# Kernel tuning notes

Hardware: AMD Instinct MI355X
Metric: run time of the kernel (lower is better)

The kernel has to match this reference:

```python
import jax, jax.numpy as jnp
import numpy as np

D_MODEL = 5
NUM_PRED = 3
D_K = D_MODEL + NUM_PRED  # 8
HIDDEN = 128
GRID_LEN = 0.1
NUM_GRIDS = 100  # time_horizon / grid_length
SCALE = float(np.power(D_K, 0.5))
OH = np.eye(NUM_PRED, dtype=np.float32)
ONEHOT_M = jnp.asarray(OH[0])   # mental predicate 0
ONEHOT_A1 = jnp.asarray(OH[1])  # action predicate 1
ONEHOT_A2 = jnp.asarray(OH[2])  # action predicate 2


def time_emb(t):
    # positional-style embedding: even dims sin, odd dims cos (matches fast_time_embedding)
    i = jnp.arange(D_MODEL)
    ang = jnp.asarray(t)[..., None] / (10000.0 ** (2.0 * i / D_MODEL))
    return jnp.where(i % 2 == 0, jnp.sin(ang), jnp.cos(ang))


def setup_inputs() -> dict:
    key = jax.random.key(0)
    ks = jax.random.split(key, 11)
    B, L = 1024, 2048
    times_a1 = jnp.sort(jax.random.uniform(ks[0], (B, L)) * 10.0, axis=1)
    times_a2 = jnp.sort(jax.random.uniform(ks[1], (B, L)) * 10.0, axis=1)
    u = jax.random.uniform(ks[2], (B, NUM_GRIDS))
    s = 0.05
    return {
        'times_a1': times_a1,
        'times_a2': times_a2,
        'u': u,
        'W_ih': s * jax.random.normal(ks[3], (4 * HIDDEN, 21)),
        'W_hh': s * jax.random.normal(ks[4], (4 * HIDDEN, HIDDEN)),
        'b_ih': s * jax.random.normal(ks[5], (4 * HIDDEN,)),
        'b_hh': s * jax.random.normal(ks[6], (4 * HIDDEN,)),
        'w1': s * jax.random.normal(ks[7], (5, HIDDEN)),
        'b1': s * jax.random.normal(ks[8], (5,)),
        'w2': s * jax.random.normal(ks[9], (1, 5)),
        'b2': s * jax.random.normal(ks[10], (1,)),
    }


def _forward(times_a1, times_a2, u, W_ih, W_hh, b_ih, b_hh, w1, b1, w2, b2):
    B = times_a1.shape[0]
    # action event embeddings: [B, L, D_MODEL+NUM_PRED]; k = v = concat over action types
    e1 = jnp.concatenate([time_emb(times_a1), jnp.broadcast_to(ONEHOT_A1, times_a1.shape + (NUM_PRED,))], axis=-1)
    e2 = jnp.concatenate([time_emb(times_a2), jnp.broadcast_to(ONEHOT_A2, times_a2.shape + (NUM_PRED,))], axis=-1)
    kv = jnp.concatenate([e1, e2], axis=1)  # [B, 2L, 8]

    cur_times = (jnp.arange(NUM_GRIDS) + 1.0) * GRID_LEN  # [100]

    def step(carry, xs):
        hx, cx, last_time, has_event, dyn_time = carry
        cur_time, u_t = xs
        # query for mental predicate 0 at cur_time: [8]
        q = jnp.concatenate([time_emb(cur_time), ONEHOT_M])
        scores = jnp.einsum('d,bld->bl', q, kv) / SCALE
        attn = jax.nn.softmax(scores, axis=-1)
        att_out = jnp.einsum('bl,bld->bd', attn, kv)  # [B, 8]
        # mental embedding: zeros before first event, else time-emb of last event + one-hot
        m_emb = jnp.concatenate([time_emb(last_time), jnp.broadcast_to(ONEHOT_M, (B, NUM_PRED))], axis=-1)
        m_emb = jnp.where(has_event[:, None], m_emb, 0.0)
        dyn_time = dyn_time + GRID_LEN
        ct_emb = time_emb(dyn_time)  # [B, 5]
        x = jnp.concatenate([att_out, m_emb, ct_emb], axis=-1)  # [B, 21]
        # torch LSTMCell: gates ordered i, f, g, o
        gates = x @ W_ih.T + hx @ W_hh.T + b_ih + b_hh
        i_, f_, g_, o_ = jnp.split(gates, 4, axis=-1)
        cx = jax.nn.sigmoid(f_) * cx + jax.nn.sigmoid(i_) * jnp.tanh(g_)
        hx = jax.nn.sigmoid(o_) * jnp.tanh(cx)
        hz = jax.nn.sigmoid((hx @ w1.T + b1) @ w2.T + b2)[:, 0]  # [B]
        # bernoulli(prob) with pre-drawn uniform; single mental predicate -> index always 0
        event = u_t < hz
        last_time = jnp.where(event, cur_time, last_time)
        has_event = has_event | event
        dyn_time = jnp.where(event, 0.0, dyn_time)
        return (hx, cx, last_time, has_event, dyn_time), (hz, event)

    init = (
        jnp.zeros((B, HIDDEN)), jnp.zeros((B, HIDDEN)),
        jnp.zeros((B,)), jnp.zeros((B,), dtype=bool), jnp.zeros((B,)),
    )
    _, (hazard, events) = jax.lax.scan(step, init, (cur_times, u.T))
    return hazard, events  # [NUM_GRIDS, B], [NUM_GRIDS, B]


def reference(times_a1, times_a2, u, W_ih, W_hh, b_ih, b_hh, w1, b1, w2, b2):
    return _forward(times_a1, times_a2, u, W_ih, W_hh, b_ih, b_hh, w1, b1, w2, b2)
```

## Files before the change

### kernel.cpp

```cpp
#include <hip/hip_runtime.h>
#include <math.h>

#define BTOT 1024
#define LEN  2048
#define T    100
#define HID  128

#define C1 0.025118864315095794
#define C2 6.309573444801933e-04
#define C3 1.5848931924611134e-05
#define C4 3.9810717055349735e-07

#define TEMB(td) \
  float d0 = sinf((float)(td)); \
  float d1 = cosf((float)((td) * C1)); \
  float d2 = sinf((float)((td) * C2)); \
  float d3 = cosf((float)((td) * C3)); \
  float d4 = sinf((float)((td) * C4));

__device__ __forceinline__ float sig(float x) { return 1.0f / (1.0f + expf(-x)); }

using v2f = __attribute__((ext_vector_type(2))) float;
__device__ __forceinline__ v2f mkv2(float a, float b) { v2f r; r.x = a; r.y = b; return r; }

template <int CTRL>
__device__ __forceinline__ float dppadd(float x) {
  int r = __builtin_amdgcn_update_dpp(0, __float_as_int(x), CTRL, 0xF, 0xF, false);
  return x + __int_as_float(r);
}
__device__ __forceinline__ float wred(float x) {
  x = dppadd<0xB1>(x);
  x = dppadd<0x4E>(x);
  x = dppadd<0x124>(x);
  x = dppadd<0x128>(x);
  x += __shfl_xor(x, 16);
  x += __shfl_xor(x, 32);
  return x;
}
#define RED4(x) { x = dppadd<0xB1>(x); x = dppadd<0x4E>(x); }

#define AGSTASH(a_, v_) asm volatile("v_accvgpr_write_b32 %0, %1" : "=a"(a_) : "v"(v_))
#define AGREAD(v_, a_)  asm volatile("v_accvgpr_read_b32 %0, %1" : "=v"(v_) : "a"(a_))

__global__ __attribute__((amdgpu_flat_work_group_size(512, 512)))
void attn_k(const float* __restrict__ ta1,
            const float* __restrict__ ta2,
            float* __restrict__ att) {
  const int b = blockIdx.x, tid = threadIdx.x;
  const int wave = tid >> 6, lane = tid & 63;

  __shared__ float qlds[T][8];
  __shared__ float strip[8][T][8];

  if (tid < T) {
    double ct = (double)(tid + 1) * 0.1;
    TEMB(ct);
    qlds[tid][0] = d0 * 0.35355339059327373f;
    qlds[tid][1] = d1 * 0.35355339059327373f;
    qlds[tid][2] = d2 * 0.35355339059327373f;
    qlds[tid][3] = d3 * 0.35355339059327373f;
    qlds[tid][4] = d4 * 0.35355339059327373f;
  }

#define E5(i) float e##i##_0, e##i##_1, e##i##_2, e##i##_3, e##i##_4;
  E5(0) E5(1) E5(2) E5(3) E5(4) E5(5) E5(6) E5(7)
#undef E5
#define STAGE(i, expr) { double td_ = (double)(expr); \
    e##i##_0 = sinf((float)td_); \
    e##i##_1 = cosf((float)(td_ * C1)); \
    e##i##_2 = sinf((float)(td_ * C2)); \
    e##i##_3 = cosf((float)(td_ * C3)); \
    e##i##_4 = sinf((float)(td_ * C4)); }
  STAGE(0, ta1[b * LEN + tid +    0])
  STAGE(1, ta1[b * LEN + tid +  512])
  STAGE(2, ta1[b * LEN + tid + 1024])
  STAGE(3, ta1[b * LEN + tid + 1536])
  STAGE(4, ta2[b * LEN + tid +    0])
  STAGE(5, ta2[b * LEN + tid +  512])
  STAGE(6, ta2[b * LEN + tid + 1024])
  STAGE(7, ta2[b * LEN + tid + 1536])
#undef STAGE
#define PIN5(i) asm volatile("" : "+v"(e##i##_0), "+v"(e##i##_1), \
    "+v"(e##i##_2), "+v"(e##i##_3), "+v"(e##i##_4));
  PIN5(0) PIN5(1) PIN5(2) PIN5(3) PIN5(4) PIN5(5) PIN5(6) PIN5(7)
#undef PIN5

  __syncthreads();

  for (int t = 0; t < T; t++) {
    const float4 qv = *(const float4*)&qlds[t][0];
    const float q4 = qlds[t][4];
    float Wx = 0.f, Wy = 0.f, Wz = 0.f, Ww = 0.f, W4 = 0.f, sA = 0.f, sB = 0.f;
#define EV(i, S) { \
    float s = fmaf(qv.x, e##i##_0, fmaf(qv.y, e##i##_1, \
              fmaf(qv.z, e##i##_2, fmaf(qv.w, e##i##_3, q4 * e##i##_4)))); \
    float e = __expf(s); S += e; \
    Wx = fmaf(e, e##i##_0, Wx); Wy = fmaf(e, e##i##_1, Wy); \
    Wz = fmaf(e, e##i##_2, Wz); Ww = fmaf(e, e##i##_3, Ww); \
    W4 = fmaf(e, e##i##_4, W4); }
    EV(0, sA) EV(1, sA) EV(2, sA) EV(3, sA)
    EV(4, sB) EV(5, sB) EV(6, sB) EV(7, sB)
#undef EV

    float r0 = wred(Wx), r1 = wred(Wy), r2 = wred(Wz), r3 = wred(Ww);
    float r4 = wred(W4), r5 = wred(sA), r6 = wred(sB);
    if (lane == 0) {
      *(float4*)&strip[wave][t][0] = make_float4(r0, r1, r2, r3);
      strip[wave][t][4] = r4; strip[wave][t][5] = r5; strip[wave][t][6] = r6;
    }
  }
  __syncthreads();

  if (tid < T) {
    float f0 = 0.f, f1 = 0.f, f2 = 0.f, f3 = 0.f, f4 = 0.f, f5 = 0.f, f6 = 0.f;
#pragma unroll
    for (int w = 0; w < 8; w++) {
      float4 a = *(float4*)&strip[w][tid][0];
      float4 bq = *(float4*)&strip[w][tid][4];
      f0 += a.x; f1 += a.y; f2 += a.z; f3 += a.w;
      f4 += bq.x; f5 += bq.y; f6 += bq.z;
    }
    float inv = 1.0f / (f5 + f6);
    float* o8 = &att[(size_t)b * (T * 8) + (size_t)tid * 8];
    o8[0] = f0 * inv; o8[1] = f1 * inv; o8[2] = f2 * inv;
    o8[3] = f3 * inv; o8[4] = f4 * inv;
    o8[5] = 0.f; o8[6] = f5 * inv; o8[7] = f6 * inv;
  }
}

#define XE(tb, b, e) (((tb) * 4 + (b)) * 160 + (e))

__global__ __attribute__((amdgpu_flat_work_group_size(512, 512), amdgpu_waves_per_eu(2, 4)))
void lstm_k(const float* __restrict__ att,
            const float* __restrict__ u,
            const float* __restrict__ Wih,
            const float* __restrict__ Whh,
            const float* __restrict__ bih,
            const float* __restrict__ bhh,
            const float* __restrict__ w1g,
            const float* __restrict__ b1g,
            const float* __restrict__ w2g,
            const float* __restrict__ b2g,
            float* __restrict__ out) {
  const int tid = threadIdx.x;
  const int bg = blockIdx.x * 4;
  const int q = tid >> 2, s = tid & 3;
  const int lane = tid & 63;
  const int s10 = s * 10;

  __shared__ float4 xls4[2][4][40];
  __shared__ float4 glds[4][128];
  __shared__ float red2[4][2];
  __shared__ float tembT[101][5];
  __shared__ float uT[4][100];
  __shared__ int stL[2][4], stD[2][4], stH[2][4];
  float* xf = (float*)xls4;

#define DECL4(g, c) float agw##g##_##c##_0, agw##g##_##c##_1, agw##g##_##c##_2, agw##g##_##c##_3;
  DECL4(0,0) DECL4(0,1) DECL4(0,2) DECL4(0,3) DECL4(0,4) DECL4(0,5) DECL4(0,6) DECL4(0,7) DECL4(0,8) DECL4(0,9)
  DECL4(1,0) DECL4(1,1) DECL4(1,2) DECL4(1,3) DECL4(1,4) DECL4(1,5) DECL4(1,6) DECL4(1,7) DECL4(1,8) DECL4(1,9)
  DECL4(2,0) DECL4(2,1) DECL4(2,2) DECL4(2,3) DECL4(2,4) DECL4(2,5) DECL4(2,6) DECL4(2,7) DECL4(2,8) DECL4(2,9)
  DECL4(3,0) DECL4(3,1) DECL4(3,2) DECL4(3,3) DECL4(3,4) DECL4(3,5) DECL4(3,6) DECL4(3,7) DECL4(3,8) DECL4(3,9)
#undef DECL4
#define LD4(g, c) { \
    int E_ = 40 * s + 4 * (c); \
    float4 wv4_; \
    if (E_ >= 24 && E_ < 152) { \
      wv4_ = *(const float4*)(Whh + (size_t)(q + 128 * (g)) * HID + (E_ - 24)); \
    } else if (E_ < 24) { \
      wv4_.x = (E_ + 0 < 21) ? Wih[(q + 128 * (g)) * 21 + E_ + 0] : 0.f; \
      wv4_.y = (E_ + 1 < 21) ? Wih[(q + 128 * (g)) * 21 + E_ + 1] : 0.f; \
      wv4_.z = (E_ + 2 < 21) ? Wih[(q + 128 * (g)) * 21 + E_ + 2] : 0.f; \
      wv4_.w = (E_ + 3 < 21) ? Wih[(q + 128 * (g)) * 21 + E_ + 3] : 0.f; \
    } else { wv4_ = make_float4(0.f, 0.f, 0.f, 0.f); } \
    AGSTASH(agw##g##_##c##_0, wv4_.x); AGSTASH(agw##g##_##c##_1, wv4_.y); \
    AGSTASH(agw##g##_##c##_2, wv4_.z); AGSTASH(agw##g##_##c##_3, wv4_.w); }
  LD4(0,0) LD4(0,1) LD4(0,2) LD4(0,3) LD4(0,4) LD4(0,5) LD4(0,6) LD4(0,7) LD4(0,8) LD4(0,9)
  LD4(1,0) LD4(1,1) LD4(1,2) LD4(1,3) LD4(1,4) LD4(1,5) LD4(1,6) LD4(1,7) LD4(1,8) LD4(1,9)
  LD4(2,0) LD4(2,1) LD4(2,2) LD4(2,3) LD4(2,4) LD4(2,5) LD4(2,6) LD4(2,7) LD4(2,8) LD4(2,9)
  LD4(3,0) LD4(3,1) LD4(3,2) LD4(3,3) LD4(3,4) LD4(3,5) LD4(3,6) LD4(3,7) LD4(3,8) LD4(3,9)
#undef LD4

  const int chI = tid & 127;
  float bbc0 = bih[chI] + bhh[chI];
  float bbc1 = bih[chI + 128] + bhh[chI + 128];
  float bbc2 = bih[chI + 256] + bhh[chI + 256];
  float bbc3 = bih[chI + 384] + bhh[chI + 384];
  float wvc = 0.f;
#pragma unroll
  for (int j = 0; j < 5; j++) wvc = fmaf(w2g[j], w1g[j * HID + chI], wvc);
  float hconst = b2g[0];
#pragma unroll
  for (int j = 0; j < 5; j++) hconst = fmaf(w2g[j], b1g[j], hconst);
  asm volatile("" : "+v"(bbc0), "+v"(bbc1), "+v"(bbc2), "+v"(bbc3),
                    "+v"(wvc), "+v"(hconst));
  float cx = 0.f;

  for (int i = tid; i < 2 * 4 * 160; i += 512) xf[i] = 0.f;
  if (tid < 101) {
    double td = (double)tid * 0.1;
    TEMB(td);
    tembT[tid][0] = d0; tembT[tid][1] = d1; tembT[tid][2] = d2;
    tembT[tid][3] = d3; tembT[tid][4] = d4;
  }
  for (int i = tid; i < 400; i += 512) {
    int b = i / 100, tt = i - b * 100;
    uT[b][tt] = u[(size_t)(bg + b) * T + tt];
  }
  if (tid < 4) { stL[0][tid] = 0; stD[0][tid] = 0; stH[0][tid] = 0; }
  __syncthreads();

  if (tid < 32) {
    int b = tid >> 3, j = tid & 7;
    xf[XE(0, b, j)] = att[(size_t)(bg + b) * (T * 8) + j];
  } else if (tid >= 64 && tid < 84) {
    int s2 = tid - 64, b = s2 / 5, j = s2 % 5;
    xf[XE(0, b, 16 + j)] = tembT[1][j];
  }
  __syncthreads();

#define GFMA(g, c) { \
    float t0_, t1_, t2_, t3_; \
    AGREAD(t0_, agw##g##_##c##_0); AGREAD(t1_, agw##g##_##c##_1); \
    AGREAD(t2_, agw##g##_##c##_2); AGREAD(t3_, agw##g##_##c##_3); \
    v2f wlo_ = mkv2(t0_, t1_), whi_ = mkv2(t2_, t3_); \
    a##g##0 = __builtin_elementwise_fma(wlo_, x0lo, a##g##0); \
    a##g##0 = __builtin_elementwise_fma(whi_, x0hi, a##g##0); \
    a##g##1 = __builtin_elementwise_fma(wlo_, x1lo, a##g##1); \
    a##g##1 = __builtin_elementwise_fma(whi_, x1hi, a##g##1); \
    a##g##2 = __builtin_elementwise_fma(wlo_, x2lo, a##g##2); \
    a##g##2 = __builtin_elementwise_fma(whi_, x2hi, a##g##2); \
    a##g##3 = __builtin_elementwise_fma(wlo_, x3lo, a##g##3); \
    a##g##3 = __builtin_elementwise_fma(whi_, x3hi, a##g##3); }

#define CH(c) { \
    float4 xb0_ = xls4[tb][0][s10 + (c)], xb1_ = xls4[tb][1][s10 + (c)], \
           xb2_ = xls4[tb][2][s10 + (c)], xb3_ = xls4[tb][3][s10 + (c)]; \
    v2f x0lo = mkv2(xb0_.x, xb0_.y), x0hi = mkv2(xb0_.z, xb0_.w); \
    v2f x1lo = mkv2(xb1_.x, xb1_.y), x1hi = mkv2(xb1_.z, xb1_.w); \
    v2f x2lo = mkv2(xb2_.x, xb2_.y), x2hi = mkv2(xb2_.z, xb2_.w); \
    v2f x3lo = mkv2(xb3_.x, xb3_.y), x3hi = mkv2(xb3_.z, xb3_.w); \
    GFMA(0, c) GFMA(1, c) GFMA(2, c) GFMA(3, c) }

#define CALCEV(bb) \
    float z_ = hconst + red2[bb][0] + red2[bb][1]; \
    float hz_ = 1.f / (1.f + expf(-z_)); \
    int ev_ = (uT[bb][t] < hz_) ? 1 : 0; \
    int lastp_ = ev_ ? (t + 1) : stL[tb][bb]; \
    int hasp_ = stH[tb][bb] | ev_; \
    int dynp_ = ev_ ? 0 : (stD[tb][bb] + 1);

  for (int t = 0; t < T; t++) {
    const int tb = t & 1, tb1 = tb ^ 1;

    v2f z2 = mkv2(0.f, 0.f);
    v2f a00 = z2, a01 = z2, a02 = z2, a03 = z2,
        a10 = z2, a11 = z2, a12 = z2, a13 = z2,
        a20 = z2, a21 = z2, a22 = z2, a23 = z2,
        a30 = z2, a31 = z2, a32 = z2, a33 = z2;
    CH(0) CH(1) CH(2) CH(3) CH(4) CH(5) CH(6) CH(7) CH(8) CH(9)

    float h00 = a00.x + a00.y, h01 = a01.x + a01.y, h02 = a02.x + a02.y, h03 = a03.x + a03.y;
    float h10 = a10.x + a10.y, h11 = a11.x + a11.y, h12 = a12.x + a12.y, h13 = a13.x + a13.y;
    float h20 = a20.x + a20.y, h21 = a21.x + a21.y, h22 = a22.x + a22.y, h23 = a23.x + a23.y;
    float h30 = a30.x + a30.y, h31 = a31.x + a31.y, h32 = a32.x + a32.y, h33 = a33.x + a33.y;
    RED4(h00) RED4(h01) RED4(h02) RED4(h03)
    RED4(h10) RED4(h11) RED4(h12) RED4(h13)
    RED4(h20) RED4(h21) RED4(h22) RED4(h23)
    RED4(h30) RED4(h31) RED4(h32) RED4(h33)
    if (s == 0) {
      glds[0][q] = make_float4(h00, h10, h20, h30);
      glds[1][q] = make_float4(h01, h11, h21, h31);
      glds[2][q] = make_float4(h02, h12, h22, h32);
      glds[3][q] = make_float4(h03, h13, h23, h33);
    }
    __syncthreads();

    {
      int b = tid >> 7;
      float4 g4 = glds[b][chI];
      float gi = g4.x + bbc0, gf = g4.y + bbc1, gG = g4.z + bbc2, go = g4.w + bbc3;
      cx = sig(gf) * cx + sig(gi) * tanhf(gG);
      float hn = sig(go) * tanhf(cx);
      xf[XE(tb1, b, 24 + chI)] = hn;
      float pb = wred(wvc * hn);
      if (lane == 0) red2[b][(tid >> 6) & 1] = pb;
    }
    __syncthreads();

    if (tid < 4) {
      int b = tid;
      CALCEV(b);
      out[(size_t)t * BTOT + bg + b] = hz_;
      out[(size_t)T * BTOT + (size_t)t * BTOT + bg + b] = ev_ ? 1.f : 0.f;
      stL[tb1][b] = lastp_; stH[tb1][b] = hasp_; stD[tb1][b] = dynp_;
    }
    if (t < T - 1) {
      if (tid < 32) {
        int b = tid >> 3, j = tid & 7;
        xf[XE(tb1, b, j)] = att[(size_t)(bg + b) * (T * 8) + (size_t)(t + 1) * 8 + j];
      } else if (tid < 52) {
        int s2 = tid - 32, b = s2 / 5, j = s2 % 5;
        CALCEV(b);
        xf[XE(tb1, b, 8 + j)] = hasp_ ? tembT[lastp_][j] : 0.f;
      } else if (tid < 64) {
        int s2 = tid - 52, b = s2 / 3, j = s2 % 3;
        CALCEV(b);
        xf[XE(tb1, b, 13 + j)] = (j == 0 && hasp_) ? 1.f : 0.f;
      } else if (tid < 84) {
        int s2 = tid - 64, b = s2 / 5, j = s2 % 5;
        CALCEV(b);
        xf[XE(tb1, b, 16 + j)] = tembT[dynp_ + 1][j];
      }
    }
    __syncthreads();
  }
#undef CALCEV
#undef CH
#undef GFMA
}

extern "C" void kernel_launch(void* const* d_in, const int* in_sizes, int n_in,
                              void* d_out, int out_size, void* d_ws, size_t ws_size,
                              hipStream_t stream) {
  const float* ta1 = (const float*)d_in[0];
  const float* ta2 = (const float*)d_in[1];
  const float* u   = (const float*)d_in[2];
  const float* Wih = (const float*)d_in[3];
  const float* Whh = (const float*)d_in[4];
  const float* bih = (const float*)d_in[5];
  const float* bhh = (const float*)d_in[6];
  const float* w1  = (const float*)d_in[7];
  const float* b1  = (const float*)d_in[8];
  const float* w2  = (const float*)d_in[9];
  const float* b2  = (const float*)d_in[10];
  float* out = (float*)d_out;
  float* att = (float*)d_ws;

  attn_k<<<dim3(BTOT), dim3(512), 0, stream>>>(ta1, ta2, att);
  lstm_k<<<dim3(BTOT / 4), dim3(512), 0, stream>>>(att, u, Wih, Whh, bih, bhh,
                                                   w1, b1, w2, b2, out);
}
```

Before: 729.1 us.

## Halve batch rows per LSTM block and overlap next-step input load

Each LSTM workgroup now processes 2 batch rows instead of 4, doubling the number of workgroups so the serial recurrence spreads over more compute units with less FMA work per step. The loads of the next step's attention input move into otherwise idle threads during the gate-activation phase. The waves_per_eu hint is removed. In exchange, weight loading into registers is repeated across twice as many blocks, and occupancy depends on whether two blocks fit per CU.

Result: slower. 917.9 us (+25.9%).

```diff
diff --git a/kernel.cpp b/kernel.cpp
--- a/kernel.cpp
+++ b/kernel.cpp
@@ -5,6 +5,7 @@
 #define LEN  2048
 #define T    100
 #define HID  128
+#define BPW  2
 
 #define C1 0.025118864315095794
 #define C2 6.309573444801933e-04
@@ -128,9 +129,9 @@
   }
 }
 
-#define XE(tb, b, e) (((tb) * 4 + (b)) * 160 + (e))
-
-__global__ __attribute__((amdgpu_flat_work_group_size(512, 512), amdgpu_waves_per_eu(2, 4)))
+#define XE(tb, b, e) (((tb) * BPW + (b)) * 160 + (e))
+
+__global__ __attribute__((amdgpu_flat_work_group_size(512, 512)))
 void lstm_k(const float* __restrict__ att,
             const float* __restrict__ u,
             const float* __restrict__ Wih,
@@ -143,17 +144,17 @@
             const float* __restrict__ b2g,
             float* __restrict__ out) {
   const int tid = threadIdx.x;
-  const int bg = blockIdx.x * 4;
+  const int bg = blockIdx.x * BPW;
   const int q = tid >> 2, s = tid & 3;
   const int lane = tid & 63;
   const int s10 = s * 10;
 
-  __shared__ float4 xls4[2][4][40];
-  __shared__ float4 glds[4][128];
-  __shared__ float red2[4][2];
+  __shared__ float4 xls4[2][BPW][40];
+  __shared__ float4 glds[BPW][128];
+  __shared__ float red2[BPW][2];
   __shared__ float tembT[101][5];
-  __shared__ float uT[4][100];
-  __shared__ int stL[2][4], stD[2][4], stH[2][4];
+  __shared__ float uT[BPW][100];
+  __shared__ int stL[2][BPW], stD[2][BPW], stH[2][BPW];
   float* xf = (float*)xls4;
 
 #define DECL4(g, c) float agw##g##_##c##_0, agw##g##_##c##_1, agw##g##_##c##_2, agw##g##_##c##_3;
@@ -196,24 +197,24 @@
                     "+v"(wvc), "+v"(hconst));
   float cx = 0.f;
 
-  for (int i = tid; i < 2 * 4 * 160; i += 512) xf[i] = 0.f;
+  for (int i = tid; i < 2 * BPW * 160; i += 512) xf[i] = 0.f;
   if (tid < 101) {
     double td = (double)tid * 0.1;
     TEMB(td);
     tembT[tid][0] = d0; tembT[tid][1] = d1; tembT[tid][2] = d2;
     tembT[tid][3] = d3; tembT[tid][4] = d4;
   }
-  for (int i = tid; i < 400; i += 512) {
+  for (int i = tid; i < BPW * 100; i += 512) {
     int b = i / 100, tt = i - b * 100;
     uT[b][tt] = u[(size_t)(bg + b) * T + tt];
   }
-  if (tid < 4) { stL[0][tid] = 0; stD[0][tid] = 0; stH[0][tid] = 0; }
+  if (tid < BPW) { stL[0][tid] = 0; stD[0][tid] = 0; stH[0][tid] = 0; }
   __syncthreads();
 
-  if (tid < 32) {
+  if (tid < BPW * 8) {
     int b = tid >> 3, j = tid & 7;
     xf[XE(0, b, j)] = att[(size_t)(bg + b) * (T * 8) + j];
-  } else if (tid >= 64 && tid < 84) {
+  } else if (tid >= 64 && tid < 64 + BPW * 5) {
     int s2 = tid - 64, b = s2 / 5, j = s2 % 5;
     xf[XE(0, b, 16 + j)] = tembT[1][j];
   }
@@ -227,19 +228,12 @@
     a##g##0 = __builtin_elementwise_fma(wlo_, x0lo, a##g##0); \
     a##g##0 = __builtin_elementwise_fma(whi_, x0hi, a##g##0); \
     a##g##1 = __builtin_elementwise_fma(wlo_, x1lo, a##g##1); \
-    a##g##1 = __builtin_elementwise_fma(whi_, x1hi, a##g##1); \
-    a##g##2 = __builtin_elementwise_fma(wlo_, x2lo, a##g##2); \
-    a##g##2 = __builtin_elementwise_fma(whi_, x2hi, a##g##2); \
-    a##g##3 = __builtin_elementwise_fma(wlo_, x3lo, a##g##3); \
-    a##g##3 = __builtin_elementwise_fma(whi_, x3hi, a##g##3); }
+    a##g##1 = __builtin_elementwise_fma(whi_, x1hi, a##g##1); }
 
 #define CH(c) { \
-    float4 xb0_ = xls4[tb][0][s10 + (c)], xb1_ = xls4[tb][1][s10 + (c)], \
-           xb2_ = xls4[tb][2][s10 + (c)], xb3_ = xls4[tb][3][s10 + (c)]; \
+    float4 xb0_ = xls4[tb][0][s10 + (c)], xb1_ = xls4[tb][1][s10 + (c)]; \
     v2f x0lo = mkv2(xb0_.x, xb0_.y), x0hi = mkv2(xb0_.z, xb0_.w); \
     v2f x1lo = mkv2(xb1_.x, xb1_.y), x1hi = mkv2(xb1_.z, xb1_.w); \
-    v2f x2lo = mkv2(xb2_.x, xb2_.y), x2hi = mkv2(xb2_.z, xb2_.w); \
-    v2f x3lo = mkv2(xb3_.x, xb3_.y), x3hi = mkv2(xb3_.z, xb3_.w); \
     GFMA(0, c) GFMA(1, c) GFMA(2, c) GFMA(3, c) }
 
 #define CALCEV(bb) \
@@ -254,29 +248,25 @@
     const int tb = t & 1, tb1 = tb ^ 1;
 
     v2f z2 = mkv2(0.f, 0.f);
-    v2f a00 = z2, a01 = z2, a02 = z2, a03 = z2,
-        a10 = z2, a11 = z2, a12 = z2, a13 = z2,
-        a20 = z2, a21 = z2, a22 = z2, a23 = z2,
-        a30 = z2, a31 = z2, a32 = z2, a33 = z2;
+    v2f a00 = z2, a01 = z2,
+        a10 = z2, a11 = z2,
+        a20 = z2, a21 = z2,
+        a30 = z2, a31 = z2;
     CH(0) CH(1) CH(2) CH(3) CH(4) CH(5) CH(6) CH(7) CH(8) CH(9)
 
-    float h00 = a00.x + a00.y, h01 = a01.x + a01.y, h02 = a02.x + a02.y, h03 = a03.x + a03.y;
-    float h10 = a10.x + a10.y, h11 = a11.x + a11.y, h12 = a12.x + a12.y, h13 = a13.x + a13.y;
-    float h20 = a20.x + a20.y, h21 = a21.x + a21.y, h22 = a22.x + a22.y, h23 = a23.x + a23.y;
-    float h30 = a30.x + a30.y, h31 = a31.x + a31.y, h32 = a32.x + a32.y, h33 = a33.x + a33.y;
-    RED4(h00) RED4(h01) RED4(h02) RED4(h03)
-    RED4(h10) RED4(h11) RED4(h12) RED4(h13)
-    RED4(h20) RED4(h21) RED4(h22) RED4(h23)
-    RED4(h30) RED4(h31) RED4(h32) RED4(h33)
+    float h00 = a00.x + a00.y, h01 = a01.x + a01.y;
+    float h10 = a10.x + a10.y, h11 = a11.x + a11.y;
+    float h20 = a20.x + a20.y, h21 = a21.x + a21.y;
+    float h30 = a30.x + a30.y, h31 = a31.x + a31.y;
+    RED4(h00) RED4(h01) RED4(h10) RED4(h11)
+    RED4(h20) RED4(h21) RED4(h30) RED4(h31)
     if (s == 0) {
       glds[0][q] = make_float4(h00, h10, h20, h30);
       glds[1][q] = make_float4(h01, h11, h21, h31);
-      glds[2][q] = make_float4(h02, h12, h22, h32);
-      glds[3][q] = make_float4(h03, h13, h23, h33);
     }
     __syncthreads();
 
-    {
+    if (tid < 256) {
       int b = tid >> 7;
       float4 g4 = glds[b][chI];
       float gi = g4.x + bbc0, gf = g4.y + bbc1, gG = g4.z + bbc2, go = g4.w + bbc3;
@@ -285,10 +275,13 @@
       xf[XE(tb1, b, 24 + chI)] = hn;
       float pb = wred(wvc * hn);
       if (lane == 0) red2[b][(tid >> 6) & 1] = pb;
+    } else if (tid < 256 + BPW * 8 && t < T - 1) {
+      int s2 = tid - 256, b = s2 >> 3, j = s2 & 7;
+      xf[XE(tb1, b, j)] = att[(size_t)(bg + b) * (T * 8) + (size_t)(t + 1) * 8 + j];
     }
     __syncthreads();
 
-    if (tid < 4) {
+    if (tid < BPW) {
       int b = tid;
       CALCEV(b);
       out[(size_t)t * BTOT + bg + b] = hz_;
@@ -296,18 +289,15 @@
       stL[tb1][b] = lastp_; stH[tb1][b] = hasp_; stD[tb1][b] = dynp_;
     }
     if (t < T - 1) {
-      if (tid < 32) {
-        int b = tid >> 3, j = tid & 7;
-        xf[XE(tb1, b, j)] = att[(size_t)(bg + b) * (T * 8) + (size_t)(t + 1) * 8 + j];
-      } else if (tid < 52) {
+      if (tid >= 32 && tid < 32 + BPW * 5) {
         int s2 = tid - 32, b = s2 / 5, j = s2 % 5;
         CALCEV(b);
         xf[XE(tb1, b, 8 + j)] = hasp_ ? tembT[lastp_][j] : 0.f;
-      } else if (tid < 64) {
+      } else if (tid >= 52 && tid < 52 + BPW * 3) {
         int s2 = tid - 52, b = s2 / 3, j = s2 % 3;
         CALCEV(b);
         xf[XE(tb1, b, 13 + j)] = (j == 0 && hasp_) ? 1.f : 0.f;
-      } else if (tid < 84) {
+      } else if (tid >= 64 && tid < 64 + BPW * 5) {
         int s2 = tid - 64, b = s2 / 5, j = s2 % 5;
         CALCEV(b);
         xf[XE(tb1, b, 16 + j)] = tembT[dynp_ + 1][j];
@@ -338,6 +328,6 @@
   float* att = (float*)d_ws;
 
   attn_k<<<dim3(BTOT), dim3(512), 0, stream>>>(ta1, ta2, att);
-  lstm_k<<<dim3(BTOT / 4), dim3(512), 0, stream>>>(att, u, Wih, Whh, bih, bhh,
-                                                   w1, b1, w2, b2, out);
-}
+  lstm_k<<<dim3(BTOT / BPW), dim3(512), 0, stream>>>(att, u, Wih, Whh, bih, bhh,
+                                                     w1, b1, w2, b2, out);
+}
```

## Map each batch row to one wave in LSTM cell update to drop a barrier

Applied to the files above, without the earlier changes.

Reworks the per-step LSTM cell update so each of the first four waves owns one batch row and handles two hidden channels per lane. The hazard reduction becomes a full-wave reduction, and the event state (last time, has-event, dynamic time) is kept in registers instead of shared memory. This removes one block barrier per time step and the separate single-thread event stage. The trade-off is that only half the threads do the elementwise work, each with twice the transcendental calls, while the other waves idle apart from loading the attention inputs for the next step.

Measured after the change: 705.6 us. -3.2%, faster.

```diff
diff --git a/kernel.cpp b/kernel.cpp
--- a/kernel.cpp
+++ b/kernel.cpp
@@ -5,6 +5,7 @@
 #define LEN  2048
 #define T    100
 #define HID  128
+#define BPW  4
 
 #define C1 0.025118864315095794
 #define C2 6.309573444801933e-04
@@ -33,6 +34,15 @@
   x = dppadd<0x4E>(x);
   x = dppadd<0x124>(x);
   x = dppadd<0x128>(x);
+  x += __shfl_xor(x, 16);
+  x += __shfl_xor(x, 32);
+  return x;
+}
+__device__ __forceinline__ float wredall(float x) {
+  x = dppadd<0xB1>(x);
+  x = dppadd<0x4E>(x);
+  x = dppadd<0x141>(x);
+  x += __shfl_xor(x, 8);
   x += __shfl_xor(x, 16);
   x += __shfl_xor(x, 32);
   return x;
@@ -128,7 +138,7 @@
   }
 }
 
-#define XE(tb, b, e) (((tb) * 4 + (b)) * 160 + (e))
+#define XE(tb, b, e) (((tb) * BPW + (b)) * 160 + (e))
 
 __global__ __attribute__((amdgpu_flat_work_group_size(512, 512), amdgpu_waves_per_eu(2, 4)))
 void lstm_k(const float* __restrict__ att,
@@ -143,18 +153,26 @@
             const float* __restrict__ b2g,
             float* __restrict__ out) {
   const int tid = threadIdx.x;
-  const int bg = blockIdx.x * 4;
+  const int bg = blockIdx.x * BPW;
   const int q = tid >> 2, s = tid & 3;
-  const int lane = tid & 63;
   const int s10 = s * 10;
 
-  __shared__ float4 xls4[2][4][40];
-  __shared__ float4 glds[4][128];
-  __shared__ float red2[4][2];
+  __shared__ float4 xls4[2][BPW][40];
+  __shared__ float4 glds[BPW][128];
   __shared__ float tembT[101][5];
-  __shared__ float uT[4][100];
-  __shared__ int stL[2][4], stD[2][4], stH[2][4];
+  __shared__ float uT[BPW][100];
   float* xf = (float*)xls4;
+
+#define LOADW(g, c, dstv) { \
+    int E_ = 40 * s + 4 * (c); \
+    if (E_ >= 24 && E_ < 152) { \
+      dstv = *(const float4*)(Whh + (size_t)(q + 128 * (g)) * HID + (E_ - 24)); \
+    } else if (E_ < 24) { \
+      dstv.x = (E_ + 0 < 21) ? Wih[(q + 128 * (g)) * 21 + E_ + 0] : 0.f; \
+      dstv.y = (E_ + 1 < 21) ? Wih[(q + 128 * (g)) * 21 + E_ + 1] : 0.f; \
+      dstv.z = (E_ + 2 < 21) ? Wih[(q + 128 * (g)) * 21 + E_ + 2] : 0.f; \
+      dstv.w = (E_ + 3 < 21) ? Wih[(q + 128 * (g)) * 21 + E_ + 3] : 0.f; \
+    } else { dstv = make_float4(0.f, 0.f, 0.f, 0.f); } }
 
 #define DECL4(g, c) float agw##g##_##c##_0, agw##g##_##c##_1, agw##g##_##c##_2, agw##g##_##c##_3;
   DECL4(0,0) DECL4(0,1) DECL4(0,2) DECL4(0,3) DECL4(0,4) DECL4(0,5) DECL4(0,6) DECL4(0,7) DECL4(0,8) DECL4(0,9)
@@ -162,17 +180,7 @@
   DECL4(2,0) DECL4(2,1) DECL4(2,2) DECL4(2,3) DECL4(2,4) DECL4(2,5) DECL4(2,6) DECL4(2,7) DECL4(2,8) DECL4(2,9)
   DECL4(3,0) DECL4(3,1) DECL4(3,2) DECL4(3,3) DECL4(3,4) DECL4(3,5) DECL4(3,6) DECL4(3,7) DECL4(3,8) DECL4(3,9)
 #undef DECL4
-#define LD4(g, c) { \
-    int E_ = 40 * s + 4 * (c); \
-    float4 wv4_; \
-    if (E_ >= 24 && E_ < 152) { \
-      wv4_ = *(const float4*)(Whh + (size_t)(q + 128 * (g)) * HID + (E_ - 24)); \
-    } else if (E_ < 24) { \
-      wv4_.x = (E_ + 0 < 21) ? Wih[(q + 128 * (g)) * 21 + E_ + 0] : 0.f; \
-      wv4_.y = (E_ + 1 < 21) ? Wih[(q + 128 * (g)) * 21 + E_ + 1] : 0.f; \
-      wv4_.z = (E_ + 2 < 21) ? Wih[(q + 128 * (g)) * 21 + E_ + 2] : 0.f; \
-      wv4_.w = (E_ + 3 < 21) ? Wih[(q + 128 * (g)) * 21 + E_ + 3] : 0.f; \
-    } else { wv4_ = make_float4(0.f, 0.f, 0.f, 0.f); } \
+#define LD4(g, c) { float4 wv4_; LOADW(g, c, wv4_); \
     AGSTASH(agw##g##_##c##_0, wv4_.x); AGSTASH(agw##g##_##c##_1, wv4_.y); \
     AGSTASH(agw##g##_##c##_2, wv4_.z); AGSTASH(agw##g##_##c##_3, wv4_.w); }
   LD4(0,0) LD4(0,1) LD4(0,2) LD4(0,3) LD4(0,4) LD4(0,5) LD4(0,6) LD4(0,7) LD4(0,8) LD4(0,9)
@@ -181,39 +189,40 @@
   LD4(3,0) LD4(3,1) LD4(3,2) LD4(3,3) LD4(3,4) LD4(3,5) LD4(3,6) LD4(3,7) LD4(3,8) LD4(3,9)
 #undef LD4
 
-  const int chI = tid & 127;
-  float bbc0 = bih[chI] + bhh[chI];
-  float bbc1 = bih[chI + 128] + bhh[chI + 128];
-  float bbc2 = bih[chI + 256] + bhh[chI + 256];
-  float bbc3 = bih[chI + 384] + bhh[chI + 384];
-  float wvc = 0.f;
+  const int cA = (tid & 63) * 2, cB = cA + 1;
+  float bA0 = bih[cA] + bhh[cA],             bB0 = bih[cB] + bhh[cB];
+  float bA1 = bih[cA + 128] + bhh[cA + 128], bB1 = bih[cB + 128] + bhh[cB + 128];
+  float bA2 = bih[cA + 256] + bhh[cA + 256], bB2 = bih[cB + 256] + bhh[cB + 256];
+  float bA3 = bih[cA + 384] + bhh[cA + 384], bB3 = bih[cB + 384] + bhh[cB + 384];
+  float wvA = 0.f, wvB = 0.f;
 #pragma unroll
-  for (int j = 0; j < 5; j++) wvc = fmaf(w2g[j], w1g[j * HID + chI], wvc);
+  for (int j = 0; j < 5; j++) {
+    wvA = fmaf(w2g[j], w1g[j * HID + cA], wvA);
+    wvB = fmaf(w2g[j], w1g[j * HID + cB], wvB);
+  }
   float hconst = b2g[0];
 #pragma unroll
   for (int j = 0; j < 5; j++) hconst = fmaf(w2g[j], b1g[j], hconst);
-  asm volatile("" : "+v"(bbc0), "+v"(bbc1), "+v"(bbc2), "+v"(bbc3),
-                    "+v"(wvc), "+v"(hconst));
-  float cx = 0.f;
-
-  for (int i = tid; i < 2 * 4 * 160; i += 512) xf[i] = 0.f;
+  float cxA = 0.f, cxB = 0.f;
+  int lastp = 0, hasp = 0, dynp = 0;
+
+  for (int i = tid; i < 2 * BPW * 160; i += 512) xf[i] = 0.f;
   if (tid < 101) {
     double td = (double)tid * 0.1;
     TEMB(td);
     tembT[tid][0] = d0; tembT[tid][1] = d1; tembT[tid][2] = d2;
     tembT[tid][3] = d3; tembT[tid][4] = d4;
   }
-  for (int i = tid; i < 400; i += 512) {
+  for (int i = tid; i < BPW * 100; i += 512) {
     int b = i / 100, tt = i - b * 100;
     uT[b][tt] = u[(size_t)(bg + b) * T + tt];
   }
-  if (tid < 4) { stL[0][tid] = 0; stD[0][tid] = 0; stH[0][tid] = 0; }
   __syncthreads();
 
-  if (tid < 32) {
+  if (tid < BPW * 8) {
     int b = tid >> 3, j = tid & 7;
     xf[XE(0, b, j)] = att[(size_t)(bg + b) * (T * 8) + j];
-  } else if (tid >= 64 && tid < 84) {
+  } else if (tid >= 64 && tid < 64 + BPW * 5) {
     int s2 = tid - 64, b = s2 / 5, j = s2 % 5;
     xf[XE(0, b, 16 + j)] = tembT[1][j];
   }
@@ -241,14 +250,6 @@
     v2f x2lo = mkv2(xb2_.x, xb2_.y), x2hi = mkv2(xb2_.z, xb2_.w); \
     v2f x3lo = mkv2(xb3_.x, xb3_.y), x3hi = mkv2(xb3_.z, xb3_.w); \
     GFMA(0, c) GFMA(1, c) GFMA(2, c) GFMA(3, c) }
-
-#define CALCEV(bb) \
-    float z_ = hconst + red2[bb][0] + red2[bb][1]; \
-    float hz_ = 1.f / (1.f + expf(-z_)); \
-    int ev_ = (uT[bb][t] < hz_) ? 1 : 0; \
-    int lastp_ = ev_ ? (t + 1) : stL[tb][bb]; \
-    int hasp_ = stH[tb][bb] | ev_; \
-    int dynp_ = ev_ ? 0 : (stD[tb][bb] + 1);
 
   for (int t = 0; t < T; t++) {
     const int tb = t & 1, tb1 = tb ^ 1;
@@ -276,48 +277,36 @@
     }
     __syncthreads();
 
-    {
-      int b = tid >> 7;
-      float4 g4 = glds[b][chI];
-      float gi = g4.x + bbc0, gf = g4.y + bbc1, gG = g4.z + bbc2, go = g4.w + bbc3;
-      cx = sig(gf) * cx + sig(gi) * tanhf(gG);
-      float hn = sig(go) * tanhf(cx);
-      xf[XE(tb1, b, 24 + chI)] = hn;
-      float pb = wred(wvc * hn);
-      if (lane == 0) red2[b][(tid >> 6) & 1] = pb;
+    if (tid < 256) {
+      const int w = tid >> 6, l = tid & 63;
+      float4 gA = glds[w][cA], gB = glds[w][cB];
+      cxA = sig(gA.y + bA1) * cxA + sig(gA.x + bA0) * tanhf(gA.z + bA2);
+      float hnA = sig(gA.w + bA3) * tanhf(cxA);
+      cxB = sig(gB.y + bB1) * cxB + sig(gB.x + bB0) * tanhf(gB.z + bB2);
+      float hnB = sig(gB.w + bB3) * tanhf(cxB);
+      *(float2*)&xf[XE(tb1, w, 24 + cA)] = make_float2(hnA, hnB);
+      float pb = wredall(fmaf(wvA, hnA, wvB * hnB));
+      float hz = 1.f / (1.f + expf(-(hconst + pb)));
+      int ev = (uT[w][t] < hz) ? 1 : 0;
+      lastp = ev ? (t + 1) : lastp;
+      hasp |= ev;
+      dynp = ev ? 0 : (dynp + 1);
+      if (l == 0) out[(size_t)t * BTOT + bg + w] = hz;
+      if (l == 1) out[(size_t)T * BTOT + (size_t)t * BTOT + bg + w] = ev ? 1.f : 0.f;
+      if (t < T - 1) {
+        if (l < 5)        xf[XE(tb1, w, 8 + l)] = hasp ? tembT[lastp][l] : 0.f;
+        else if (l < 8)   xf[XE(tb1, w, 13 + (l - 5))] = (l == 5 && hasp) ? 1.f : 0.f;
+        else if (l < 13)  xf[XE(tb1, w, 16 + (l - 8))] = tembT[dynp + 1][l - 8];
+      }
+    } else if (tid < 256 + BPW * 8 && t < T - 1) {
+      int s2 = tid - 256, b = s2 >> 3, j = s2 & 7;
+      xf[XE(tb1, b, j)] = att[(size_t)(bg + b) * (T * 8) + (size_t)(t + 1) * 8 + j];
     }
     __syncthreads();
-
-    if (tid < 4) {
-      int b = tid;
-      CALCEV(b);
-      out[(size_t)t * BTOT + bg + b] = hz_;
-      out[(size_t)T * BTOT + (size_t)t * BTOT + bg + b] = ev_ ? 1.f : 0.f;
-      stL[tb1][b] = lastp_; stH[tb1][b] = hasp_; stD[tb1][b] = dynp_;
-    }
-    if (t < T - 1) {
-      if (tid < 32) {
-        int b = tid >> 3, j = tid & 7;
-        xf[XE(tb1, b, j)] = att[(size_t)(bg + b) * (T * 8) + (size_t)(t + 1) * 8 + j];
-      } else if (tid < 52) {
-        int s2 = tid - 32, b = s2 / 5, j = s2 % 5;
-        CALCEV(b);
-        xf[XE(tb1, b, 8 + j)] = hasp_ ? tembT[lastp_][j] : 0.f;
-      } else if (tid < 64) {
-        int s2 = tid - 52, b = s2 / 3, j = s2 % 3;
-        CALCEV(b);
-        xf[XE(tb1, b, 13 + j)] = (j == 0 && hasp_) ? 1.f : 0.f;
-      } else if (tid < 84) {
-        int s2 = tid - 64, b = s2 / 5, j = s2 % 5;
-        CALCEV(b);
-        xf[XE(tb1, b, 16 + j)] = tembT[dynp_ + 1][j];
-      }
-    }
-    __syncthreads();
-  }
-#undef CALCEV
+  }
 #undef CH
 #undef GFMA
+#undef LOADW
 }
 
 extern "C" void kernel_launch(void* const* d_in, const int* in_sizes, int n_in,
@@ -338,6 +327,6 @@
   float* att = (float*)d_ws;
 
   attn_k<<<dim3(BTOT), dim3(512), 0, stream>>>(ta1, ta2, att);
-  lstm_k<<<dim3(BTOT / 4), dim3(512), 0, stream>>>(att, u, Wih, Whh, bih, bhh,
-                                                   w1, b1, w2, b2, out);
-}
+  lstm_k<<<dim3(BTOT / BPW), dim3(512), 0, stream>>>(att, u, Wih, Whh, bih, bhh,
+                                                     w1, b1, w2, b2, out);
+}
```
